# Performance work log

Hardware: AMD Instinct MI355X
Metric: run time of the kernel (lower is better)

The kernel has to match this reference:

```python
import math
import jax, jax.numpy as jnp
import numpy as np

D = 512; H = 8; DH = 64          # d_model, heads, head dim
AB = 8                            # attention block size (BigBird block)
NG, NW, NR = 2, 5, 3              # global / window / random blocks
K = NG + NW + NR                  # attended blocks per query block
NL = 5                            # layers per (encoder|decoder) stack
MAXSEQ = 1024; BS = 4; NM = 4; LAT = 16; FF = 2048


def setup_inputs() -> dict:
    key = jax.random.key(0)
    ks = jax.random.split(key, 20)
    B = 32
    S_enc = MAXSEQ + 1
    nb_enc = (S_enc + AB - 1) // AB   # 129
    nb_dec = MAXSEQ // AB             # 128
    def n(i, shape, s=0.02):
        return jax.random.normal(ks[i], shape, jnp.float32) * s
    return {
        'x': jax.random.normal(ks[0], (B, MAXSEQ, BS * NM), jnp.float32),
        'eps': jax.random.normal(ks[1], (B, LAT), jnp.float32),
        'emb_in': n(2, (S_enc, D)),
        'emb_out': n(3, (MAXSEQ, D)),
        'W_data': n(4, (BS * NM, D)), 'b_data': jnp.zeros((D,), jnp.float32),
        'Wqkv': n(5, (2 * NL, D, 3 * D)), 'bqkv': jnp.zeros((2 * NL, 3 * D), jnp.float32),
        'Wo': n(6, (2 * NL, D, D)), 'bo': jnp.zeros((2 * NL, D), jnp.float32),
        'ln1_g': jnp.ones((2 * NL, D), jnp.float32), 'ln1_b': jnp.zeros((2 * NL, D), jnp.float32),
        'W1': n(7, (2 * NL, D, FF)), 'b1': jnp.zeros((2 * NL, FF), jnp.float32),
        'W2': n(8, (2 * NL, FF, D)), 'b2': jnp.zeros((2 * NL, D), jnp.float32),
        'ln2_g': jnp.ones((2 * NL, D), jnp.float32), 'ln2_b': jnp.zeros((2 * NL, D), jnp.float32),
        'W_mean': n(9, (D, LAT)), 'b_mean': jnp.zeros((LAT,), jnp.float32),
        'W_lv': n(10, (D, LAT)), 'b_lv': jnp.zeros((LAT,), jnp.float32),
        'W_exp': n(11, (LAT, 2 * MAXSEQ)), 'b_exp': jnp.zeros((2 * MAXSEQ,), jnp.float32),
        'W_conv': n(12, (2, D)), 'b_conv': jnp.zeros((D,), jnp.float32),
        'W_seq': n(13, (D, BS * NM)), 'b_seq': jnp.zeros((BS * NM,), jnp.float32),
        'rand_enc': jax.random.randint(ks[14], (nb_enc, NR), 0, nb_enc, jnp.int32),
        'rand_dec': jax.random.randint(ks[15], (nb_dec, NR), 0, nb_dec, jnp.int32),
    }


def _ln(x, g, b):
    m = jnp.mean(x, -1, keepdims=True)
    v = jnp.var(x, -1, keepdims=True)
    return (x - m) * jax.lax.rsqrt(v + 1e-5) * g + b


def _block_index(nb, rand):
    # per query block: NG global blocks, NW window blocks, NR random blocks
    i = jnp.arange(nb)
    g = jnp.broadcast_to(jnp.arange(NG)[None, :], (nb, NG))
    w = i[:, None] + (jnp.arange(NW) - NW // 2)[None, :]
    w_valid = (w >= 0) & (w < nb)
    idx = jnp.concatenate([g, jnp.clip(w, 0, nb - 1), rand], axis=1)          # [nb, K]
    valid = jnp.concatenate([jnp.ones((nb, NG), bool), w_valid,
                             jnp.ones((nb, NR), bool)], axis=1)               # [nb, K]
    return idx, valid


def _sparse_attn(x, Wqkv, bqkv, Wo, bo, rand):
    # BigBird-style block-sparse self attention (global + window + random blocks)
    B, S, _ = x.shape
    nb = (S + AB - 1) // AB
    Sp = nb * AB
    qkv = jnp.pad(x @ Wqkv + bqkv, ((0, 0), (0, Sp - S), (0, 0)))
    q, k, v = jnp.split(qkv, 3, axis=-1)
    def blk(t):  # [B,Sp,D] -> [B,H,nb,AB,DH]
        return t.reshape(B, nb, AB, H, DH).transpose(0, 3, 1, 2, 4)
    q, k, v = blk(q), blk(k), blk(v)
    idx, bvalid = _block_index(nb, rand)
    kg = k[:, :, idx]                      # [B,H,nb,K,AB,DH]
    vg = v[:, :, idx]
    scores = jnp.einsum('bhnqd,bhnkpd->bhnqkp', q, kg) / math.sqrt(DH)  # [B,H,nb,AB,K,AB]
    tok_valid = (jnp.arange(Sp) < S).reshape(nb, AB)
    kmask = bvalid[:, :, None] & tok_valid[idx]                          # [nb,K,AB]
    scores = jnp.where(kmask[None, None, :, None], scores, -1e9)
    attn = jax.nn.softmax(scores.reshape(B, H, nb, AB, K * AB), axis=-1)
    out = jnp.einsum('bhnqk,bhnkd->bhnqd', attn, vg.reshape(B, H, nb, K * AB, DH))
    out = out.transpose(0, 2, 3, 1, 4).reshape(B, Sp, D)[:, :S]
    return out @ Wo + bo


def _layer(x, i, p, rand):
    (Wqkv, bqkv, Wo, bo, ln1_g, ln1_b, W1, b1, W2, b2, ln2_g, ln2_b) = p
    a = _sparse_attn(x, Wqkv[i], bqkv[i], Wo[i], bo[i], rand)
    x = _ln(x + a, ln1_g[i], ln1_b[i])
    f = jax.nn.relu(x @ W1[i] + b1[i]) @ W2[i] + b2[i]
    return _ln(x + f, ln2_g[i], ln2_b[i])


def _forward(x, eps, emb_in, emb_out, W_data, b_data, Wqkv, bqkv, Wo, bo,
             ln1_g, ln1_b, W1, b1, W2, b2, ln2_g, ln2_b, W_mean, b_mean,
             W_lv, b_lv, W_exp, b_exp, W_conv, b_conv, W_seq, b_seq,
             rand_enc, rand_dec):
    B = x.shape[0]
    p = (Wqkv, bqkv, Wo, bo, ln1_g, ln1_b, W1, b1, W2, b2, ln2_g, ln2_b)
    # ---- encode ----
    h = x @ W_data + b_data                                   # [B,1024,512]
    cls = jnp.zeros((B, 1, D), x.dtype)
    h = jnp.concatenate([cls, h], axis=1) + emb_in            # [B,1025,512]
    for i in range(NL):
        h = _layer(h, i, p, rand_enc)
    pooled = h[:, 0]
    mean = pooled @ W_mean + b_mean
    logvar = pooled @ W_lv + b_lv
    # ---- sample (diag-Gaussian rsample) ----
    z = mean + eps * jnp.exp(0.5 * logvar)
    # ---- decode ----
    seq = (z @ W_exp + b_exp).reshape(B, 2, MAXSEQ)           # [B,2,1024]
    d = jnp.einsum('bcs,cd->bsd', seq, W_conv) + b_conv       # 1x1 conv, -> [B,1024,512]
    d = d + emb_out
    for i in range(NL, 2 * NL):
        d = _layer(d, i, p, rand_dec)
    out = d @ W_seq + b_seq                                   # [B,1024,16] (1x1 conv)
    decoded = out.reshape(B, -1, NM)                          # [B,4096,4]
    elbo = jnp.mean(-0.5 * jnp.sum(1.0 + logvar - mean ** 2 - jnp.exp(logvar), axis=1))
    return decoded, elbo


def reference(x, eps, emb_in, emb_out, W_data, b_data, Wqkv, bqkv, Wo, bo,
              ln1_g, ln1_b, W1, b1, W2, b2, ln2_g, ln2_b, W_mean, b_mean,
              W_lv, b_lv, W_exp, b_exp, W_conv, b_conv, W_seq, b_seq,
              rand_enc, rand_dec):
    return _forward(x, eps, emb_in, emb_out, W_data, b_data, Wqkv, bqkv, Wo, bo,
                    ln1_g, ln1_b, W1, b1, W2, b2, ln2_g, ln2_b, W_mean, b_mean,
                    W_lv, b_lv, W_exp, b_exp, W_conv, b_conv, W_seq, b_seq,
                    rand_enc, rand_dec)
```

## Files before the change

kernel.cpp:

```cpp
#include <hip/hip_runtime.h>

typedef unsigned short u16;
typedef __attribute__((ext_vector_type(8))) short short8;
typedef __attribute__((ext_vector_type(4))) float f32x4;

__device__ __forceinline__ float b2f(u16 h) {
  union { unsigned int u; float f; } v; v.u = ((unsigned int)h) << 16; return v.f;
}
__device__ __forceinline__ u16 f2b(float f) {
  union { float f; unsigned int u; } v; v.f = f;
  return (u16)((v.u + 0x7fffu + ((v.u >> 16) & 1u)) >> 16);
}

__device__ __forceinline__ void gload16(const u16* g, u16* l) {
  __builtin_amdgcn_global_load_lds(
      (const __attribute__((address_space(1))) void*)g,
      (__attribute__((address_space(3))) void*)l, 16, 0, 0);
}

#define SENC 1025
#define SPENC 1032
#define NBE 129
#define SDEC 1024
#define NBD 128
#define BATCH 32
#define MENC (BATCH * SPENC)
#define MDEC (BATCH * SDEC)

__global__ void beacon_k(float* out) { if (threadIdx.x == 0) out[0] = 1000.0f; }

__global__ __launch_bounds__(256) void tr_k(const float* __restrict__ W, u16* __restrict__ WT, int K, int N)
{
  __shared__ float sm[32][33];
  int k0 = blockIdx.x * 32, n0 = blockIdx.y * 32;
  const float* Wz = W + (size_t)blockIdx.z * K * N;
  u16* WTz = WT + (size_t)blockIdx.z * K * N;
  int r = threadIdx.x >> 3, c0 = (threadIdx.x & 7) * 4;
  float4 v = *(const float4*)&Wz[(size_t)(k0 + r) * N + n0 + c0];
  sm[r][c0] = v.x; sm[r][c0 + 1] = v.y; sm[r][c0 + 2] = v.z; sm[r][c0 + 3] = v.w;
  __syncthreads();
  ushort4 u;
  u.x = f2b(sm[c0][r]); u.y = f2b(sm[c0 + 1][r]); u.z = f2b(sm[c0 + 2][r]); u.w = f2b(sm[c0 + 3][r]);
  *(ushort4*)&WTz[(size_t)(n0 + r) * K + k0 + c0] = u;
}

__global__ __launch_bounds__(256) void embed_k(const float* __restrict__ x, const float* __restrict__ Wd,
    const float* __restrict__ bd, const float* __restrict__ emb, float* __restrict__ h, u16* __restrict__ hb)
{
  size_t gid = (size_t)blockIdx.x * 256 + threadIdx.x;
  int dd = (int)(gid & 511);
  size_t rs = gid >> 9;
  int s = (int)(rs % SPENC);
  int b = (int)(rs / SPENC);
  float v;
  if (s == 0) {
    v = emb[dd];
  } else if (s < SENC) {
    float acc = bd[dd];
    const float* xr = x + ((size_t)b * 1024 + (s - 1)) * 16;
    #pragma unroll
    for (int j = 0; j < 16; ++j) acc += xr[j] * Wd[j * 512 + dd];
    v = acc + emb[(size_t)s * 512 + dd];
  } else {
    v = 0.f;
  }
  h[gid] = v;
  hb[gid] = f2b(v);
}

template<bool RELU>
__global__ __launch_bounds__(512) void mgemm_k(const u16* __restrict__ A, const u16* __restrict__ WT,
    const float* __restrict__ bias, u16* __restrict__ C,
    int M, int N, int Kc, int lda, int ldb)
{
  __shared__ __align__(16) u16 sA[3][128 * 32];
  __shared__ __align__(16) u16 sB[3][256 * 32];
  int t = threadIdx.x;

  int gx = gridDim.x;
  int nwg = gx * gridDim.y;
  int flat = blockIdx.y * gx + blockIdx.x;
  int q = nwg >> 3, rr = nwg & 7;
  int xcd = flat & 7, idx = flat >> 3;
  int swz = (xcd < rr ? xcd * (q + 1) : rr * (q + 1) + (xcd - rr) * q) + idx;
  int bx = swz % gx, by = swz / gx;

  int n0 = bx * 256, m0 = by * 128;
  int lane = t & 63, wave = t >> 6;
  int wm = (wave >> 2) * 64, wn = (wave & 3) * 64;
  int quad = lane >> 4, l15 = lane & 15;

  int rA = t >> 2, sc = t & 3;
  int cA = sc ^ ((rA >> 1) & 3);
  int raA = m0 + rA; raA = raA < M ? raA : M - 1;
  const u16* gA  = A  + (size_t)raA * lda + cA * 8;
  const u16* gB0 = WT + (size_t)(n0 + rA) * ldb + cA * 8;
  const u16* gB1 = WT + (size_t)(n0 + 128 + rA) * ldb + cA * 8;

  f32x4 acc[4][4];
  #pragma unroll
  for (int i = 0; i < 4; ++i)
    #pragma unroll
    for (int j = 0; j < 4; ++j) acc[i][j] = (f32x4){0.f, 0.f, 0.f, 0.f};

  const int nt = Kc >> 5;
  gload16(gA,      &sA[0][t * 8]);
  gload16(gB0,     &sB[0][t * 8]);
  gload16(gB1,     &sB[0][(512 + t) * 8]);
  gload16(gA + 32, &sA[1][t * 8]);
  gload16(gB0 + 32,&sB[1][t * 8]);
  gload16(gB1 + 32,&sB[1][(512 + t) * 8]);

  int cur = 0;
  for (int tt = 0; tt < nt; ++tt) {
    if (tt < nt - 1) {
      asm volatile("s_waitcnt vmcnt(3)" ::: "memory");
    } else {
      asm volatile("s_waitcnt vmcnt(0)" ::: "memory");
    }
    __builtin_amdgcn_s_barrier();
    asm volatile("" ::: "memory");
    if (tt + 2 < nt) {
      int k0 = (tt + 2) << 5;
      int nb = tt + 2; nb -= (nb / 3) * 3;
      gload16(gA + k0,  &sA[nb][t * 8]);
      gload16(gB0 + k0, &sB[nb][t * 8]);
      gload16(gB1 + k0, &sB[nb][(512 + t) * 8]);
    }
    short8 af[4], bf[4];
    #pragma unroll
    for (int i = 0; i < 4; ++i) {
      int ra = wm + i * 16 + l15;
      af[i] = *(const short8*)&sA[cur][ra * 32 + (quad ^ ((ra >> 1) & 3)) * 8];
    }
    #pragma unroll
    for (int j = 0; j < 4; ++j) {
      int rb = wn + j * 16 + l15;
      bf[j] = *(const short8*)&sB[cur][rb * 32 + (quad ^ ((rb >> 1) & 3)) * 8];
    }
    __builtin_amdgcn_s_setprio(1);
    #pragma unroll
    for (int i = 0; i < 4; ++i)
      #pragma unroll
      for (int j = 0; j < 4; ++j)
        acc[i][j] = __builtin_amdgcn_mfma_f32_16x16x32_bf16(af[i], bf[j], acc[i][j], 0, 0, 0);
    __builtin_amdgcn_s_setprio(0);
    cur = (cur == 2) ? 0 : cur + 1;
  }

  #pragma unroll
  for (int i = 0; i < 4; ++i) {
    int mBase = m0 + wm + i * 16 + quad * 4;
    #pragma unroll
    for (int r = 0; r < 4; ++r) {
      int m = mBase + r;
      if (m < M) {
        #pragma unroll
        for (int j = 0; j < 4; ++j) {
          int n = n0 + wn + j * 16 + l15;
          float v = acc[i][j][r] + bias[n];
          if (RELU) v = fmaxf(v, 0.f);
          C[(size_t)m * N + n] = f2b(v);
        }
      }
    }
  }
}

__global__ __launch_bounds__(256) void lnf_k(float* __restrict__ h, const u16* __restrict__ tmp,
    u16* __restrict__ hb, const float* __restrict__ g, const float* __restrict__ bb)
{
  __shared__ float ls[4], lq[4];
  int t = threadIdx.x;
  float* p = h + (size_t)blockIdx.x * 512;
  const u16* tp = tmp + (size_t)blockIdx.x * 512;
  u16* pb = hb + (size_t)blockIdx.x * 512;
  float2 hv = *(const float2*)&p[2 * t];
  ushort2 tv = *(const ushort2*)&tp[2 * t];
  float v0 = hv.x + b2f(tv.x);
  float v1 = hv.y + b2f(tv.y);
  float s = v0 + v1, qq = v0 * v0 + v1 * v1;
  #pragma unroll
  for (int off = 1; off < 64; off <<= 1) {
    s += __shfl_xor(s, off);
    qq += __shfl_xor(qq, off);
  }
  if ((t & 63) == 0) { ls[t >> 6] = s; lq[t >> 6] = qq; }
  __syncthreads();
  s = ls[0] + ls[1] + ls[2] + ls[3];
  qq = lq[0] + lq[1] + lq[2] + lq[3];
  float mean = s * (1.f / 512.f);
  float var = fmaxf(qq * (1.f / 512.f) - mean * mean, 0.f);
  float rinv = rsqrtf(var + 1e-5f);
  float o0 = (v0 - mean) * rinv * g[2 * t] + bb[2 * t];
  float o1 = (v1 - mean) * rinv * g[2 * t + 1] + bb[2 * t + 1];
  *(float2*)&p[2 * t] = make_float2(o0, o1);
  ushort2 ob; ob.x = f2b(o0); ob.y = f2b(o1);
  *(ushort2*)&pb[2 * t] = ob;
}

__global__ __launch_bounds__(64) void attnm_k(const u16* __restrict__ qkv, u16* __restrict__ av,
    const int* __restrict__ rnd, int S, int Sp, int nb)
{
  __shared__ __align__(16) u16 Vt[64 * 104];
  __shared__ __align__(16) u16 Pl[16 * 104];
  __shared__ int sJB[10], sVD[10];
  int t = threadIdx.x;
  int n = blockIdx.x % nb;
  int r1 = blockIdx.x / nb;
  int hh = r1 & 7, b = r1 >> 3;
  const u16* base = qkv + (size_t)b * Sp * 1536;
  int l15 = t & 15, quad = t >> 4;

  if (t < 10) {
    int jb, vd;
    if (t < 2) { jb = t; vd = 1; }
    else if (t < 7) {
      int w = n + t - 4;
      vd = (w >= 0 && w < nb) ? 1 : 0;
      jb = w < 0 ? 0 : (w > nb - 1 ? nb - 1 : w);
    } else { jb = rnd[n * 3 + t - 7]; vd = 1; }
    sJB[t] = jb; sVD[t] = vd;
  }
  {
    f32x4 zz = {0.f, 0.f, 0.f, 0.f};
    *(f32x4*)&Vt[t * 104 + 80] = zz;
    *(f32x4*)&Vt[t * 104 + 88] = zz;
    if (t < 16) {
      *(f32x4*)&Pl[t * 104 + 80] = zz;
      *(f32x4*)&Pl[t * 104 + 88] = zz;
    }
  }
  __syncthreads();

  short8 aq0, aq1;
  {
    const u16* qp = base + (size_t)(n * 8 + (l15 & 7)) * 1536 + hh * 64 + quad * 8;
    aq0 = *(const short8*)qp;
    aq1 = *(const short8*)(qp + 32);
  }

  f32x4 s[5];
  float okm[5];
  #pragma unroll
  for (int tile = 0; tile < 5; ++tile) {
    int kb = tile * 2 + (l15 >> 3);
    int tok = sJB[kb] * 8 + (l15 & 7);
    okm[tile] = (sVD[kb] && tok < S) ? 0.f : -3.0e38f;
    const u16* kp = base + (size_t)tok * 1536 + 512 + hh * 64 + quad * 8;
    short8 k0 = *(const short8*)kp;
    short8 k1 = *(const short8*)(kp + 32);
    f32x4 c = {0.f, 0.f, 0.f, 0.f};
    c = __builtin_amdgcn_mfma_f32_16x16x32_bf16(aq0, k0, c, 0, 0, 0);
    c = __builtin_amdgcn_mfma_f32_16x16x32_bf16(aq1, k1, c, 0, 0, 0);
    s[tile] = c;
  }

  u16 vreg[80];
  #pragma unroll
  for (int vt = 0; vt < 10; ++vt) {
    const u16* vp = base + (size_t)(sJB[vt] * 8) * 1536 + 1024 + hh * 64 + t;
    #pragma unroll
    for (int j = 0; j < 8; ++j) vreg[vt * 8 + j] = vp[(size_t)j * 1536];
  }

  f32x4 mx = {-3.0e38f, -3.0e38f, -3.0e38f, -3.0e38f};
  #pragma unroll
  for (int tile = 0; tile < 5; ++tile) {
    #pragma unroll
    for (int r = 0; r < 4; ++r) {
      float v = s[tile][r] * 0.125f + okm[tile];
      s[tile][r] = v;
      mx[r] = fmaxf(mx[r], v);
    }
  }
  #pragma unroll
  for (int off = 1; off < 16; off <<= 1) {
    #pragma unroll
    for (int r = 0; r < 4; ++r) mx[r] = fmaxf(mx[r], __shfl_xor(mx[r], off));
  }
  f32x4 sm = {0.f, 0.f, 0.f, 0.f};
  #pragma unroll
  for (int tile = 0; tile < 5; ++tile) {
    #pragma unroll
    for (int r = 0; r < 4; ++r) {
      float e = __expf(s[tile][r] - mx[r]);
      s[tile][r] = e;
      sm[r] += e;
    }
  }
  #pragma unroll
  for (int off = 1; off < 16; off <<= 1) {
    #pragma unroll
    for (int r = 0; r < 4; ++r) sm[r] += __shfl_xor(sm[r], off);
  }

  #pragma unroll
  for (int tile = 0; tile < 5; ++tile)
    #pragma unroll
    for (int r = 0; r < 4; ++r)
      Pl[(quad * 4 + r) * 104 + tile * 16 + l15] = f2b(s[tile][r]);

  #pragma unroll
  for (int vt = 0; vt < 10; ++vt) {
    short8 w;
    #pragma unroll
    for (int j = 0; j < 8; ++j) ((u16*)&w)[j] = (short)vreg[vt * 8 + j];
    *(short8*)&Vt[t * 104 + vt * 8] = w;
  }
  __syncthreads();

  f32x4 o[4];
  #pragma unroll
  for (int dn = 0; dn < 4; ++dn) o[dn] = (f32x4){0.f, 0.f, 0.f, 0.f};
  #pragma unroll
  for (int ks = 0; ks < 3; ++ks) {
    short8 ap = *(const short8*)&Pl[l15 * 104 + ks * 32 + quad * 8];
    #pragma unroll
    for (int dn = 0; dn < 4; ++dn) {
      short8 bv = *(const short8*)&Vt[(dn * 16 + l15) * 104 + ks * 32 + quad * 8];
      o[dn] = __builtin_amdgcn_mfma_f32_16x16x32_bf16(ap, bv, o[dn], 0, 0, 0);
    }
  }

  if (quad < 2) {
    #pragma unroll
    for (int r = 0; r < 4; ++r) {
      int qi = quad * 4 + r;
      float inv = 1.f / sm[r];
      u16* op = av + ((size_t)b * Sp + n * 8 + qi) * 512 + hh * 64 + l15;
      #pragma unroll
      for (int dn = 0; dn < 4; ++dn)
        op[dn * 16] = f2b(o[dn][r] * inv);
    }
  }
}

__global__ __launch_bounds__(512) void head_k(const float* __restrict__ h,
    const float* __restrict__ Wm, const float* __restrict__ bm,
    const float* __restrict__ Wlv, const float* __restrict__ blv,
    const float* __restrict__ eps, float* __restrict__ z, float* out_elbo)
{
  __shared__ float red[512];
  int t = threadIdx.x;
  int b = t >> 4, i = t & 15;
  const float* p = h + (size_t)b * SPENC * 512;
  float am = bm[i], al = blv[i];
  for (int c = 0; c < 512; ++c) {
    float pv = p[c];
    am += pv * Wm[c * 16 + i];
    al += pv * Wlv[c * 16 + i];
  }
  z[t] = am + eps[t] * expf(0.5f * al);
  red[t] = -0.5f * (1.f + al - am * am - expf(al));
  __syncthreads();
  for (int o = 256; o > 0; o >>= 1) { if (t < o) red[t] += red[t + o]; __syncthreads(); }
  if (t == 0) out_elbo[0] = red[0] * (1.f / 32.f);
}

__global__ __launch_bounds__(256) void seq_k(const float* __restrict__ z, const float* __restrict__ We,
    const float* __restrict__ be, float* __restrict__ seq)
{
  int gid = blockIdx.x * 256 + threadIdx.x;
  int b = gid >> 11, c = gid & 2047;
  float acc = be[c];
  #pragma unroll
  for (int i = 0; i < 16; ++i) acc += z[b * 16 + i] * We[i * 2048 + c];
  seq[gid] = acc;
}

__global__ __launch_bounds__(256) void decinit_k(const float* __restrict__ seq, const float* __restrict__ Wc,
    const float* __restrict__ bc, const float* __restrict__ emb, float* __restrict__ h, u16* __restrict__ hb)
{
  size_t gid = (size_t)blockIdx.x * 256 + threadIdx.x;
  int dd = (int)(gid & 511);
  size_t rs = gid >> 9;
  int s = (int)(rs & 1023);
  int b = (int)(rs >> 10);
  float v = seq[b * 2048 + s] * Wc[dd] + seq[b * 2048 + 1024 + s] * Wc[512 + dd]
          + bc[dd] + emb[(size_t)s * 512 + dd];
  h[gid] = v;
  hb[gid] = f2b(v);
}

__global__ __launch_bounds__(256) void finalm_k(const u16* __restrict__ hb, const float* __restrict__ Ws,
    const float* __restrict__ bs, float* __restrict__ out)
{
  __shared__ __align__(16) u16 Wt[16 * 520];
  int t = threadIdx.x;
  for (int e = t; e < 8192; e += 256) {
    int k = e >> 4, n = e & 15;
    Wt[n * 520 + k] = f2b(Ws[e]);
  }
  __syncthreads();
  int lane = t & 63, wave = t >> 6;
  int quad = lane >> 4, l15 = lane & 15;
  int m0 = blockIdx.x * 64 + wave * 16;
  const u16* arow = hb + (size_t)(m0 + l15) * 512 + quad * 8;
  f32x4 acc = (f32x4){0.f, 0.f, 0.f, 0.f};
  #pragma unroll
  for (int ks = 0; ks < 16; ++ks) {
    short8 af = *(const short8*)(arow + ks * 32);
    short8 bf = *(const short8*)&Wt[l15 * 520 + ks * 32 + quad * 8];
    acc = __builtin_amdgcn_mfma_f32_16x16x32_bf16(af, bf, acc, 0, 0, 0);
  }
  #pragma unroll
  for (int r = 0; r < 4; ++r)
    out[(size_t)(m0 + quad * 4 + r) * 16 + l15] = acc[r] + bs[l15];
}

extern "C" void kernel_launch(void* const* d_in, const int* in_sizes, int n_in,
                              void* d_out, int out_size, void* d_ws, size_t ws_size,
                              hipStream_t stream) {
  float* out = (float*)d_out;
  (void)out_size; (void)ws_size;

  static const int EXP_DICT[30] = {
    524288, 512, 524800, 524288, 8192, 512, 7864320, 15360, 2621440, 5120,
    5120, 5120, 10485760, 20480, 10485760, 5120, 5120, 5120, 8192, 16,
    8192, 16, 32768, 2048, 1024, 512, 8192, 16, 387, 384 };
  bool dict_ok = (n_in == 30);
  if (dict_ok) for (int i = 0; i < 30; ++i) if (in_sizes[i] != EXP_DICT[i]) { dict_ok = false; break; }
  if (!dict_ok) { beacon_k<<<1, 64, 0, stream>>>(out); return; }

  const float* x      = (const float*)d_in[0];
  const float* eps    = (const float*)d_in[1];
  const float* emb_in = (const float*)d_in[2];
  const float* emb_out= (const float*)d_in[3];
  const float* W_data = (const float*)d_in[4];
  const float* b_data = (const float*)d_in[5];
  const float* Wqkv   = (const float*)d_in[6];
  const float* bqkv   = (const float*)d_in[7];
  const float* Wo     = (const float*)d_in[8];
  const float* bo     = (const float*)d_in[9];
  const float* ln1g   = (const float*)d_in[10];
  const float* ln1b   = (const float*)d_in[11];
  const float* W1     = (const float*)d_in[12];
  const float* b1     = (const float*)d_in[13];
  const float* W2     = (const float*)d_in[14];
  const float* b2     = (const float*)d_in[15];
  const float* ln2g   = (const float*)d_in[16];
  const float* ln2b   = (const float*)d_in[17];
  const float* Wm     = (const float*)d_in[18];
  const float* bm     = (const float*)d_in[19];
  const float* Wlv    = (const float*)d_in[20];
  const float* blv    = (const float*)d_in[21];
  const float* Wexp   = (const float*)d_in[22];
  const float* bexp   = (const float*)d_in[23];
  const float* Wconv  = (const float*)d_in[24];
  const float* bconv  = (const float*)d_in[25];
  const float* Wseq   = (const float*)d_in[26];
  const float* bseq   = (const float*)d_in[27];
  const int* rand_enc = (const int*)d_in[28];
  const int* rand_dec = (const int*)d_in[29];

  char* ws = (char*)d_ws;
  float* h     = (float*)ws;
  u16*   hb    = (u16*)(ws + 67633152);
  u16*   WTqkv = (u16*)(ws + 101449728);
  u16*   WTo   = (u16*)(ws + 117178368);
  u16*   WT1l  = (u16*)(ws + 122421248);
  u16*   WT2l  = (u16*)(ws + 124518400);
  u16*   qkvb  = (u16*)(ws + 126615552);
  u16*   avb   = (u16*)(ws + 126615552 + 50724864);
  u16*   tmpo  = (u16*)(ws + 126615552);
  u16*   ffnb  = (u16*)(ws + 126615552);
  u16*   tmpF  = (u16*)(ws + 126615552 + 45088768);
  float* seqb  = (float*)(ws + 194248704);
  float* z     = (float*)(ws + 194510848);

  tr_k<<<dim3(512 / 32, 1536 / 32, 10), 256, 0, stream>>>(Wqkv, WTqkv, 512, 1536);
  tr_k<<<dim3(512 / 32, 512 / 32, 10), 256, 0, stream>>>(Wo, WTo, 512, 512);

  {
    const int M = MENC;
    embed_k<<<(M * 512) / 256, 256, 0, stream>>>(x, W_data, b_data, emb_in, h, hb);
    for (int i = 0; i < 5; ++i) {
      for (int bc = 0; bc < 2; ++bc) {
        size_t roff = (size_t)bc * 16 * SPENC * 512;
        const int Mc = 16 * SPENC;
        const int ty = 129;
        mgemm_k<false><<<dim3(6, ty), 512, 0, stream>>>(
            hb + roff, WTqkv + (size_t)i * 512 * 1536, bqkv + (size_t)i * 1536, qkvb, Mc, 1536, 512, 512, 512);
        attnm_k<<<16 * 8 * NBE, 64, 0, stream>>>(qkvb, avb, rand_enc, SENC, SPENC, NBE);
        mgemm_k<false><<<dim3(2, ty), 512, 0, stream>>>(
            avb, WTo + (size_t)i * 512 * 512, bo + (size_t)i * 512, tmpo, Mc, 512, 512, 512, 512);
        lnf_k<<<Mc, 256, 0, stream>>>(h + roff, tmpo, hb + roff, ln1g + (size_t)i * 512, ln1b + (size_t)i * 512);
      }
      tr_k<<<dim3(512 / 32, 2048 / 32, 1), 256, 0, stream>>>(W1 + (size_t)i * 512 * 2048, WT1l, 512, 2048);
      tr_k<<<dim3(2048 / 32, 512 / 32, 1), 256, 0, stream>>>(W2 + (size_t)i * 2048 * 512, WT2l, 2048, 512);
      for (int cc = 0; cc < 3; ++cc) {
        size_t off = (size_t)cc * 11008;
        const int Mc = 11008;
        const int ty = 86;
        mgemm_k<true><<<dim3(8, ty), 512, 0, stream>>>(
            hb + off * 512, WT1l, b1 + (size_t)i * 2048, ffnb, Mc, 2048, 512, 512, 512);
        mgemm_k<false><<<dim3(2, ty), 512, 0, stream>>>(
            ffnb, WT2l, b2 + (size_t)i * 512, tmpF, Mc, 512, 2048, 2048, 2048);
        lnf_k<<<Mc, 256, 0, stream>>>(h + off * 512, tmpF, hb + off * 512, ln2g + (size_t)i * 512, ln2b + (size_t)i * 512);
      }
    }
  }

  head_k<<<1, 512, 0, stream>>>(h, Wm, bm, Wlv, blv, eps, z, out + 524288);
  seq_k<<<256, 256, 0, stream>>>(z, Wexp, bexp, seqb);
  decinit_k<<<(MDEC * 512) / 256, 256, 0, stream>>>(seqb, Wconv, bconv, emb_out, h, hb);

  {
    for (int i = 5; i < 10; ++i) {
      for (int bc = 0; bc < 2; ++bc) {
        size_t roff = (size_t)bc * 16 * SDEC * 512;
        const int Mc = 16 * SDEC;
        const int ty = 128;
        mgemm_k<false><<<dim3(6, ty), 512, 0, stream>>>(
            hb + roff, WTqkv + (size_t)i * 512 * 1536, bqkv + (size_t)i * 1536, qkvb, Mc, 1536, 512, 512, 512);
        attnm_k<<<16 * 8 * NBD, 64, 0, stream>>>(qkvb, avb, rand_dec, SDEC, SDEC, NBD);
        mgemm_k<false><<<dim3(2, ty), 512, 0, stream>>>(
            avb, WTo + (size_t)i * 512 * 512, bo + (size_t)i * 512, tmpo, Mc, 512, 512, 512, 512);
        lnf_k<<<Mc, 256, 0, stream>>>(h + roff, tmpo, hb + roff, ln1g + (size_t)i * 512, ln1b + (size_t)i * 512);
      }
      tr_k<<<dim3(512 / 32, 2048 / 32, 1), 256, 0, stream>>>(W1 + (size_t)i * 512 * 2048, WT1l, 512, 2048);
      tr_k<<<dim3(2048 / 32, 512 / 32, 1), 256, 0, stream>>>(W2 + (size_t)i * 2048 * 512, WT2l, 2048, 512);
      static const int DOFF[3] = {0, 11008, 22016};
      static const int DMC[3]  = {11008, 11008, 10752};
      for (int cc = 0; cc < 3; ++cc) {
        size_t off = (size_t)DOFF[cc];
        const int Mc = DMC[cc];
        const int ty = Mc / 128;
        mgemm_k<true><<<dim3(8, ty), 512, 0, stream>>>(
            hb + off * 512, WT1l, b1 + (size_t)i * 2048, ffnb, Mc, 2048, 512, 512, 512);
        mgemm_k<false><<<dim3(2, ty), 512, 0, stream>>>(
            ffnb, WT2l, b2 + (size_t)i * 512, tmpF, Mc, 512, 2048, 2048, 2048);
        lnf_k<<<Mc, 256, 0, stream>>>(h + off * 512, tmpF, hb + off * 512, ln2g + (size_t)i * 512, ln2b + (size_t)i * 512);
      }
    }
  }

  finalm_k<<<MDEC / 64, 256, 0, stream>>>(hb, Wseq, bseq, out);
}
```

Before: 6.092 ms.

## Fuse output and FFN-down GEMMs with residual add and LayerNorm

Adds a GEMM kernel whose block tile covers a full 512-wide row (128x512), so the bias, residual add and LayerNorm are done in the epilogue. It uses wave shuffles plus a small shared-memory cross-wave reduction. This removes the bf16 temporary write and read, and the separate LayerNorm launches after the attention output projection and the FFN down projection. The FFN is also rechunked from three chunks to two larger ones, reusing the freed temporary space for a bigger ffn buffer. The cost is half as many blocks for those GEMMs (one per 128 rows instead of two), lower occupancy from the larger LDS tile, and a longer serial epilogue.

Result: faster. 5.843 ms (-4.1%).

```diff
diff --git a/kernel.cpp b/kernel.cpp
--- a/kernel.cpp
+++ b/kernel.cpp
@@ -167,36 +167,120 @@
   }
 }
 
-__global__ __launch_bounds__(256) void lnf_k(float* __restrict__ h, const u16* __restrict__ tmp,
-    u16* __restrict__ hb, const float* __restrict__ g, const float* __restrict__ bb)
-{
-  __shared__ float ls[4], lq[4];
+__global__ __launch_bounds__(512) void mgemmln_k(const u16* __restrict__ A, const u16* __restrict__ WT,
+    const float* __restrict__ bias, float* __restrict__ h, u16* __restrict__ hb,
+    const float* __restrict__ g, const float* __restrict__ bbv_,
+    int M, int Kc, int lda)
+{
+  __shared__ __align__(16) u16 sA[2][128 * 32];
+  __shared__ __align__(16) u16 sB[2][512 * 32];
+  __shared__ float redS[128][4], redQ[128][4];
   int t = threadIdx.x;
-  float* p = h + (size_t)blockIdx.x * 512;
-  const u16* tp = tmp + (size_t)blockIdx.x * 512;
-  u16* pb = hb + (size_t)blockIdx.x * 512;
-  float2 hv = *(const float2*)&p[2 * t];
-  ushort2 tv = *(const ushort2*)&tp[2 * t];
-  float v0 = hv.x + b2f(tv.x);
-  float v1 = hv.y + b2f(tv.y);
-  float s = v0 + v1, qq = v0 * v0 + v1 * v1;
-  #pragma unroll
-  for (int off = 1; off < 64; off <<= 1) {
-    s += __shfl_xor(s, off);
-    qq += __shfl_xor(qq, off);
-  }
-  if ((t & 63) == 0) { ls[t >> 6] = s; lq[t >> 6] = qq; }
+  int m0 = blockIdx.x * 128;
+  int lane = t & 63, wave = t >> 6;
+  int wm = (wave >> 2) * 64, wn = (wave & 3) * 128;
+  int quad = lane >> 4, l15 = lane & 15;
+  int wnid = wave & 3;
+
+  int rA = t >> 2, sc = t & 3;
+  int cA = sc ^ ((rA >> 1) & 3);
+  const u16* gA = A + (size_t)(m0 + rA) * lda + cA * 8;
+  const u16* gB = WT + (size_t)rA * Kc + cA * 8;
+
+  f32x4 acc[4][8];
+  #pragma unroll
+  for (int i = 0; i < 4; ++i)
+    #pragma unroll
+    for (int j = 0; j < 8; ++j) acc[i][j] = (f32x4){0.f, 0.f, 0.f, 0.f};
+
+  const int nt = Kc >> 5;
+  gload16(gA, &sA[0][t * 8]);
+  #pragma unroll
+  for (int b4 = 0; b4 < 4; ++b4)
+    gload16(gB + (size_t)b4 * 128 * Kc, &sB[0][(b4 * 512 + t) * 8]);
+  int cur = 0;
+  for (int tt = 0; tt < nt; ++tt) {
+    __syncthreads();
+    if (tt + 1 < nt) {
+      int k0 = (tt + 1) << 5;
+      gload16(gA + k0, &sA[cur ^ 1][t * 8]);
+      #pragma unroll
+      for (int b4 = 0; b4 < 4; ++b4)
+        gload16(gB + (size_t)b4 * 128 * Kc + k0, &sB[cur ^ 1][(b4 * 512 + t) * 8]);
+    }
+    short8 af[4], bf[8];
+    #pragma unroll
+    for (int i = 0; i < 4; ++i) {
+      int ra = wm + i * 16 + l15;
+      af[i] = *(const short8*)&sA[cur][ra * 32 + (quad ^ ((ra >> 1) & 3)) * 8];
+    }
+    #pragma unroll
+    for (int j = 0; j < 8; ++j) {
+      int rb = wn + j * 16 + l15;
+      bf[j] = *(const short8*)&sB[cur][rb * 32 + (quad ^ ((rb >> 1) & 3)) * 8];
+    }
+    __builtin_amdgcn_s_setprio(1);
+    #pragma unroll
+    for (int i = 0; i < 4; ++i)
+      #pragma unroll
+      for (int j = 0; j < 8; ++j)
+        acc[i][j] = __builtin_amdgcn_mfma_f32_16x16x32_bf16(af[i], bf[j], acc[i][j], 0, 0, 0);
+    __builtin_amdgcn_s_setprio(0);
+    cur ^= 1;
+  }
+
+  float bsv[8];
+  #pragma unroll
+  for (int j = 0; j < 8; ++j) bsv[j] = bias[wn + j * 16 + l15];
+
+  #pragma unroll
+  for (int i = 0; i < 4; ++i) {
+    #pragma unroll
+    for (int r = 0; r < 4; ++r) {
+      int lr = wm + i * 16 + quad * 4 + r;
+      const float* hrow = h + (size_t)(m0 + lr) * 512 + wn + l15;
+      float s = 0.f, qq = 0.f;
+      #pragma unroll
+      for (int j = 0; j < 8; ++j) {
+        float v = acc[i][j][r] + bsv[j] + hrow[j * 16];
+        acc[i][j][r] = v;
+        s += v; qq += v * v;
+      }
+      #pragma unroll
+      for (int off = 1; off < 16; off <<= 1) {
+        s += __shfl_xor(s, off);
+        qq += __shfl_xor(qq, off);
+      }
+      if (l15 == 0) { redS[lr][wnid] = s; redQ[lr][wnid] = qq; }
+    }
+  }
   __syncthreads();
-  s = ls[0] + ls[1] + ls[2] + ls[3];
-  qq = lq[0] + lq[1] + lq[2] + lq[3];
-  float mean = s * (1.f / 512.f);
-  float var = fmaxf(qq * (1.f / 512.f) - mean * mean, 0.f);
-  float rinv = rsqrtf(var + 1e-5f);
-  float o0 = (v0 - mean) * rinv * g[2 * t] + bb[2 * t];
-  float o1 = (v1 - mean) * rinv * g[2 * t + 1] + bb[2 * t + 1];
-  *(float2*)&p[2 * t] = make_float2(o0, o1);
-  ushort2 ob; ob.x = f2b(o0); ob.y = f2b(o1);
-  *(ushort2*)&pb[2 * t] = ob;
+  float gv[8], bv[8];
+  #pragma unroll
+  for (int j = 0; j < 8; ++j) {
+    gv[j] = g[wn + j * 16 + l15];
+    bv[j] = bbv_[wn + j * 16 + l15];
+  }
+  #pragma unroll
+  for (int i = 0; i < 4; ++i) {
+    #pragma unroll
+    for (int r = 0; r < 4; ++r) {
+      int lr = wm + i * 16 + quad * 4 + r;
+      float s = redS[lr][0] + redS[lr][1] + redS[lr][2] + redS[lr][3];
+      float qq = redQ[lr][0] + redQ[lr][1] + redQ[lr][2] + redQ[lr][3];
+      float mean = s * (1.f / 512.f);
+      float var = fmaxf(qq * (1.f / 512.f) - mean * mean, 0.f);
+      float rinv = rsqrtf(var + 1e-5f);
+      float* hrow = h + (size_t)(m0 + lr) * 512 + wn + l15;
+      u16* hbrow = hb + (size_t)(m0 + lr) * 512 + wn + l15;
+      #pragma unroll
+      for (int j = 0; j < 8; ++j) {
+        float o = (acc[i][j][r] - mean) * rinv * gv[j] + bv[j];
+        hrow[j * 16] = o;
+        hbrow[j * 16] = f2b(o);
+      }
+    }
+  }
 }
 
 __global__ __launch_bounds__(64) void attnm_k(const u16* __restrict__ qkv, u16* __restrict__ av,
@@ -463,9 +547,7 @@
   u16*   WT2l  = (u16*)(ws + 124518400);
   u16*   qkvb  = (u16*)(ws + 126615552);
   u16*   avb   = (u16*)(ws + 126615552 + 50724864);
-  u16*   tmpo  = (u16*)(ws + 126615552);
   u16*   ffnb  = (u16*)(ws + 126615552);
-  u16*   tmpF  = (u16*)(ws + 126615552 + 45088768);
   float* seqb  = (float*)(ws + 194248704);
   float* z     = (float*)(ws + 194510848);
 
@@ -483,21 +565,21 @@
         mgemm_k<false><<<dim3(6, ty), 512, 0, stream>>>(
             hb + roff, WTqkv + (size_t)i * 512 * 1536, bqkv + (size_t)i * 1536, qkvb, Mc, 1536, 512, 512, 512);
         attnm_k<<<16 * 8 * NBE, 64, 0, stream>>>(qkvb, avb, rand_enc, SENC, SPENC, NBE);
-        mgemm_k<false><<<dim3(2, ty), 512, 0, stream>>>(
-            avb, WTo + (size_t)i * 512 * 512, bo + (size_t)i * 512, tmpo, Mc, 512, 512, 512, 512);
-        lnf_k<<<Mc, 256, 0, stream>>>(h + roff, tmpo, hb + roff, ln1g + (size_t)i * 512, ln1b + (size_t)i * 512);
+        mgemmln_k<<<ty, 512, 0, stream>>>(
+            avb, WTo + (size_t)i * 512 * 512, bo + (size_t)i * 512,
+            h + roff, hb + roff, ln1g + (size_t)i * 512, ln1b + (size_t)i * 512, Mc, 512, 512);
       }
       tr_k<<<dim3(512 / 32, 2048 / 32, 1), 256, 0, stream>>>(W1 + (size_t)i * 512 * 2048, WT1l, 512, 2048);
       tr_k<<<dim3(2048 / 32, 512 / 32, 1), 256, 0, stream>>>(W2 + (size_t)i * 2048 * 512, WT2l, 2048, 512);
-      for (int cc = 0; cc < 3; ++cc) {
-        size_t off = (size_t)cc * 11008;
-        const int Mc = 11008;
-        const int ty = 86;
+      for (int cc = 0; cc < 2; ++cc) {
+        size_t off = (size_t)cc * 16512;
+        const int Mc = 16512;
+        const int ty = 129;
         mgemm_k<true><<<dim3(8, ty), 512, 0, stream>>>(
             hb + off * 512, WT1l, b1 + (size_t)i * 2048, ffnb, Mc, 2048, 512, 512, 512);
-        mgemm_k<false><<<dim3(2, ty), 512, 0, stream>>>(
-            ffnb, WT2l, b2 + (size_t)i * 512, tmpF, Mc, 512, 2048, 2048, 2048);
-        lnf_k<<<Mc, 256, 0, stream>>>(h + off * 512, tmpF, hb + off * 512, ln2g + (size_t)i * 512, ln2b + (size_t)i * 512);
+        mgemmln_k<<<ty, 512, 0, stream>>>(
+            ffnb, WT2l, b2 + (size_t)i * 512,
+            h + off * 512, hb + off * 512, ln2g + (size_t)i * 512, ln2b + (size_t)i * 512, Mc, 2048, 2048);
       }
     }
   }
@@ -515,23 +597,21 @@
         mgemm_k<false><<<dim3(6, ty), 512, 0, stream>>>(
             hb + roff, WTqkv + (size_t)i * 512 * 1536, bqkv + (size_t)i * 1536, qkvb, Mc, 1536, 512, 512, 512);
         attnm_k<<<16 * 8 * NBD, 64, 0, stream>>>(qkvb, avb, rand_dec, SDEC, SDEC, NBD);
-        mgemm_k<false><<<dim3(2, ty), 512, 0, stream>>>(
-            avb, WTo + (size_t)i * 512 * 512, bo + (size_t)i * 512, tmpo, Mc, 512, 512, 512, 512);
-        lnf_k<<<Mc, 256, 0, stream>>>(h + roff, tmpo, hb + roff, ln1g + (size_t)i * 512, ln1b + (size_t)i * 512);
+        mgemmln_k<<<ty, 512, 0, stream>>>(
+            avb, WTo + (size_t)i * 512 * 512, bo + (size_t)i * 512,
+            h + roff, hb + roff, ln1g + (size_t)i * 512, ln1b + (size_t)i * 512, Mc, 512, 512);
       }
       tr_k<<<dim3(512 / 32, 2048 / 32, 1), 256, 0, stream>>>(W1 + (size_t)i * 512 * 2048, WT1l, 512, 2048);
       tr_k<<<dim3(2048 / 32, 512 / 32, 1), 256, 0, stream>>>(W2 + (size_t)i * 2048 * 512, WT2l, 2048, 512);
-      static const int DOFF[3] = {0, 11008, 22016};
-      static const int DMC[3]  = {11008, 11008, 10752};
-      for (int cc = 0; cc < 3; ++cc) {
-        size_t off = (size_t)DOFF[cc];
-        const int Mc = DMC[cc];
-        const int ty = Mc / 128;
+      for (int cc = 0; cc < 2; ++cc) {
+        size_t off = (size_t)cc * 16384;
+        const int Mc = 16384;
+        const int ty = 128;
         mgemm_k<true><<<dim3(8, ty), 512, 0, stream>>>(
             hb + off * 512, WT1l, b1 + (size_t)i * 2048, ffnb, Mc, 2048, 512, 512, 512);
-        mgemm_k<false><<<dim3(2, ty), 512, 0, stream>>>(
-            ffnb, WT2l, b2 + (size_t)i * 512, tmpF, Mc, 512, 2048, 2048, 2048);
-        lnf_k<<<Mc, 256, 0, stream>>>(h + off * 512, tmpF, hb + off * 512, ln2g + (size_t)i * 512, ln2b + (size_t)i * 512);
+        mgemmln_k<<<ty, 512, 0, stream>>>(
+            ffnb, WT2l, b2 + (size_t)i * 512,
+            h + off * 512, hb + off * 512, ln2g + (size_t)i * 512, ln2b + (size_t)i * 512, Mc, 2048, 2048);
       }
     }
   }
```
